# Optimization experiments

Measured on AMD Instinct MI355X. Metric: run time of the kernel, lower is better.

Reference implementation:

```python
import jax, jax.numpy as jnp
import numpy as np

D_H = 128
N_RBF = 16
R_MIN = 0.0
R_MAX = float(np.sqrt(2.0))


def _rbf(r):
    # Gaussian RBF expansion: centers linspace(R_MIN, R_MAX, N_RBF),
    # width = center spacing, exp(-(r-mu)^2 / (2*width^2))
    centers = jnp.linspace(R_MIN, R_MAX, N_RBF, dtype=r.dtype)
    width = (R_MAX - R_MIN) / (N_RBF - 1)
    gamma = 1.0 / (2.0 * width * width)
    return jnp.exp(-gamma * (r[:, None] - centers[None, :]) ** 2)


def setup_inputs() -> dict:
    key = jax.random.key(0)
    ks = jax.random.split(key, 16)
    N, E = 50000, 800000
    h = jax.random.normal(ks[0], (N, D_H), dtype=jnp.float32)
    x = jax.random.uniform(ks[1], (N, 2), dtype=jnp.float32)
    edge_index = jax.random.randint(ks[2], (2, E), 0, N, dtype=jnp.int64)
    edge_weight = jax.random.uniform(ks[3], (E,), dtype=jnp.float32)

    def lin(k, fan_in, fan_out):
        s = 1.0 / np.sqrt(fan_in)
        kw, kb = jax.random.split(k)
        W = jax.random.uniform(kw, (fan_in, fan_out), minval=-s, maxval=s, dtype=jnp.float32)
        b = jax.random.uniform(kb, (fan_out,), minval=-s, maxval=s, dtype=jnp.float32)
        return W, b

    Wm1, bm1 = lin(ks[4], 2 * D_H + N_RBF, D_H)
    Wm2, bm2 = lin(ks[5], D_H, D_H)
    Wh1, bh1 = lin(ks[6], 2 * D_H, D_H)
    Wh2, bh2 = lin(ks[7], D_H, D_H)
    ln_g = jnp.ones((D_H,), dtype=jnp.float32)
    ln_b = jnp.zeros((D_H,), dtype=jnp.float32)
    return {"h": h, "x": x, "edge_index": edge_index, "edge_weight": edge_weight,
            "Wm1": Wm1, "bm1": bm1, "Wm2": Wm2, "bm2": bm2,
            "Wh1": Wh1, "bh1": bh1, "Wh2": Wh2, "bh2": bh2,
            "ln_g": ln_g, "ln_b": ln_b}


def reference(h, x, edge_index, edge_weight, Wm1, bm1, Wm2, bm2, Wh1, bh1, Wh2, bh2, ln_g, ln_b):
    N = h.shape[0]
    src = edge_index[0]
    dst = edge_index[1]
    # per-edge geometry
    dx = x[src, :2] - x[dst, :2]                      # [E,2]
    r = jnp.sqrt(jnp.sum(dx * dx, axis=-1) + 1e-8)    # [E]
    rbf = _rbf(r)                                     # [E,n_rbf]
    # message MLP: Linear -> SiLU -> Linear
    m_in = jnp.concatenate([h[src], h[dst], rbf], axis=-1)  # [E, 2*d_h+n_rbf]
    m = jax.nn.silu(m_in @ Wm1 + bm1) @ Wm2 + bm2            # [E, d_h]
    m = m * edge_weight[:, None]
    # scatter-sum aggregate into destination nodes
    agg = jax.ops.segment_sum(m, dst, num_segments=N)        # [N, d_h]
    # node update MLP
    u_in = jnp.concatenate([h, agg], axis=-1)                # [N, 2*d_h]
    h_up = jax.nn.silu(u_in @ Wh1 + bh1) @ Wh2 + bh2         # [N, d_h]
    # residual + LayerNorm
    z = h + h_up
    mu = jnp.mean(z, axis=-1, keepdims=True)
    var = jnp.var(z, axis=-1, keepdims=True)
    return (z - mu) / jnp.sqrt(var + 1e-5) * ln_g + ln_b
```

## Files before the change

### kernel.cpp

```cpp
#include <hip/hip_runtime.h>
#include <hip/hip_bf16.h>
#include <math.h>

#define DH 128
#define NRBF 16
#define EB 256
#define NTAB 1025
#define SEGCAP 32

typedef unsigned short ushort_t;
typedef __attribute__((ext_vector_type(8))) short short8;
typedef __attribute__((ext_vector_type(4))) float floatx4;

__device__ __forceinline__ float silu_f(float v) {
    return v / (1.f + __expf(-v));
}
__device__ __forceinline__ unsigned pk_bf16(float lo, float hi) {
    __hip_bfloat162 h = __float22bfloat162_rn(make_float2(lo, hi));
    union { __hip_bfloat162 h2; unsigned u; } cv;
    cv.h2 = h;
    return cv.u;
}
__device__ __forceinline__ ushort_t f2bf1(float f) {
    unsigned u = __float_as_uint(f);
    u += 0x7FFFu + ((u >> 16) & 1u);
    return (ushort_t)(u >> 16);
}
__device__ __forceinline__ float bflo(unsigned u) { return __uint_as_float(u << 16); }
__device__ __forceinline__ float bfhi(unsigned u) { return __uint_as_float(u & 0xffff0000u); }
__device__ __forceinline__ float bf2f(ushort_t u) { return __uint_as_float(((unsigned)u) << 16); }

__device__ __forceinline__ int detect64(const int* __restrict__ ei) {
    int z = 0;
#pragma unroll
    for (int i = 0; i < 8; ++i) z |= ei[2 * i + 1];
    return (z == 0) ? 1 : 0;
}
__device__ __forceinline__ int load_dst(const int* ei, int is64, int e, int E) {
    return is64 ? ei[2 * E + 2 * e] : ei[E + e];
}
__device__ __forceinline__ int load_src(const int* ei, int is64, int e, int E) {
    return is64 ? ei[2 * e] : ei[e];
}

__global__ __launch_bounds__(256) void k_hist_prep(
    const int* __restrict__ ei, int* __restrict__ counts, int E,
    const float* __restrict__ Wm1, const float* __restrict__ Wm2,
    const float* __restrict__ Wh1, const float* __restrict__ Wh2,
    ushort_t* __restrict__ Tbf, ushort_t* __restrict__ W2f,
    ushort_t* __restrict__ W1mf, ushort_t* __restrict__ W1hf,
    ushort_t* __restrict__ W2hf, int nb_hist)
{
    const int b = blockIdx.x, tid = threadIdx.x;
    if (b < nb_hist) {
        const int e = b * 256 + tid;
        if (e < E) {
            const int is64 = detect64(ei);
            atomicAdd(&counts[load_dst(ei, is64, e, E)], 1);
        }
        return;
    }
    int b2 = b - nb_hist;
    if (b2 < 257) {
        const int i = b2 * 4 + (tid >> 6);
        if (i < NTAB) {
            const float WIDTH = 0.09428090415820634f;
            const float GAMMA = 56.25f;
            const float DELTA = 1.4142135623730951f / 1024.0f;
            const float r = (float)i * DELTA;
            const int c0 = (tid & 63) * 2;
            float a0 = 0.f, a1 = 0.f;
#pragma unroll
            for (int q = 0; q < NRBF; ++q) {
                const float dr = r - (float)q * WIDTH;
                const float w = __expf(-GAMMA * dr * dr);
                a0 = fmaf(w, Wm1[(256 + q) * DH + c0], a0);
                a1 = fmaf(w, Wm1[(256 + q) * DH + c0 + 1], a1);
            }
            *(unsigned*)(Tbf + (size_t)i * DH + c0) = pk_bf16(a0, a1);
        }
        return;
    }
    b2 -= 257;
    if (b2 < 8) {
        const int u = b2 * 256 + tid;
        const int col = u & 127, kclg = u >> 7;
        const int lg = kclg & 3, kc = kclg >> 2;
        unsigned o[4];
#pragma unroll
        for (int j = 0; j < 2; ++j) {
            o[j]     = pk_bf16(Wm2[(kc * 32 + 4 * lg + 2 * j) * DH + col],
                               Wm2[(kc * 32 + 4 * lg + 2 * j + 1) * DH + col]);
            o[2 + j] = pk_bf16(Wm2[(kc * 32 + 16 + 4 * lg + 2 * j) * DH + col],
                               Wm2[(kc * 32 + 16 + 4 * lg + 2 * j + 1) * DH + col]);
        }
        *(uint4*)(W2f + 8 * u) = make_uint4(o[0], o[1], o[2], o[3]);
        return;
    }
    b2 -= 8;
    if (b2 < 16) {
        const int u = b2 * 256 + tid;
        const int c = u & 255, kclg = u >> 8;
        const int lg = kclg & 3, kc = kclg >> 2;
        const int base = (c < 128) ? 0 : 128;
        const int cc = c & 127;
        unsigned o[4];
#pragma unroll
        for (int j = 0; j < 2; ++j) {
            o[j]     = pk_bf16(Wm1[(base + kc * 32 + 4 * lg + 2 * j) * DH + cc],
                               Wm1[(base + kc * 32 + 4 * lg + 2 * j + 1) * DH + cc]);
            o[2 + j] = pk_bf16(Wm1[(base + kc * 32 + 16 + 4 * lg + 2 * j) * DH + cc],
                               Wm1[(base + kc * 32 + 16 + 4 * lg + 2 * j + 1) * DH + cc]);
        }
        *(uint4*)(W1mf + 8 * u) = make_uint4(o[0], o[1], o[2], o[3]);
        return;
    }
    b2 -= 16;
    if (b2 < 16) {
        const int u = b2 * 256 + tid;
        const int col = u & 127, kclg = u >> 7;
        const int lg = kclg & 3, kc = kclg >> 2;
        unsigned o[4];
#pragma unroll
        for (int j = 0; j < 2; ++j) {
            o[j]     = pk_bf16(Wh1[(kc * 32 + 4 * lg + 2 * j) * DH + col],
                               Wh1[(kc * 32 + 4 * lg + 2 * j + 1) * DH + col]);
            o[2 + j] = pk_bf16(Wh1[(kc * 32 + 16 + 4 * lg + 2 * j) * DH + col],
                               Wh1[(kc * 32 + 16 + 4 * lg + 2 * j + 1) * DH + col]);
        }
        *(uint4*)(W1hf + 8 * u) = make_uint4(o[0], o[1], o[2], o[3]);
        return;
    }
    b2 -= 16;
    {
        const int u = b2 * 256 + tid;
        const int col = u & 127, kclg = u >> 7;
        const int lg = kclg & 3, kc = kclg >> 2;
        unsigned o[4];
#pragma unroll
        for (int j = 0; j < 2; ++j) {
            o[j]     = pk_bf16(Wh2[(kc * 32 + 4 * lg + 2 * j) * DH + col],
                               Wh2[(kc * 32 + 4 * lg + 2 * j + 1) * DH + col]);
            o[2 + j] = pk_bf16(Wh2[(kc * 32 + 16 + 4 * lg + 2 * j) * DH + col],
                               Wh2[(kc * 32 + 16 + 4 * lg + 2 * j + 1) * DH + col]);
        }
        *(uint4*)(W2hf + 8 * u) = make_uint4(o[0], o[1], o[2], o[3]);
    }
}

__global__ __launch_bounds__(1024) void k_scan(const int* __restrict__ counts,
                                               int* __restrict__ cursor, int N) {
    __shared__ int wsum[16];
    __shared__ int sCarry;
    const int tid = threadIdx.x, lane = tid & 63, wid = tid >> 6;
    if (tid == 0) sCarry = 0;
    __syncthreads();
    for (int c0 = 0; c0 < N; c0 += 4096) {
        const int idx = c0 + tid * 4;
        int4 v = make_int4(0, 0, 0, 0);
        if (idx < N) v = *(const int4*)(counts + idx);
        const int t01 = v.x + v.y;
        const int t012 = t01 + v.z;
        const int tot = t012 + v.w;
        int incl = tot;
#pragma unroll
        for (int d = 1; d < 64; d <<= 1) {
            int t = __shfl_up(incl, d, 64);
            if (lane >= d) incl += t;
        }
        if (lane == 63) wsum[wid] = incl;
        __syncthreads();
        if (wid == 0) {
            int s = (lane < 16) ? wsum[lane] : 0;
#pragma unroll
            for (int d = 1; d < 16; d <<= 1) {
                int t = __shfl_up(s, d, 64);
                if (lane >= d) s += t;
            }
            if (lane < 16) wsum[lane] = s;
        }
        __syncthreads();
        const int ex = sCarry + (wid > 0 ? wsum[wid - 1] : 0) + incl - tot;
        if (idx + 3 < N) {
            *(int4*)(cursor + idx) = make_int4(ex, ex + v.x, ex + t01, ex + t012);
        } else if (idx < N) {
            cursor[idx] = ex;
            if (idx + 1 < N) cursor[idx + 1] = ex + v.x;
            if (idx + 2 < N) cursor[idx + 2] = ex + t01;
        }
        __syncthreads();
        if (tid == 0) sCarry += wsum[15];
        __syncthreads();
    }
}

__global__ __launch_bounds__(256) void k_scatter_pre(
    const int* __restrict__ ei, const float* __restrict__ ew, const float* __restrict__ x,
    int* __restrict__ cursor, uint4* __restrict__ epk,
    int E, int pack,
    const float* __restrict__ h, const float* __restrict__ bm1,
    const ushort_t* __restrict__ W1mf,
    ushort_t* __restrict__ Abf, ushort_t* __restrict__ Bbf, int N, int nb_scat)
{
    const int tid = threadIdx.x;

    if ((int)blockIdx.x < nb_scat) {
        const int e = blockIdx.x * 256 + tid;
        if (e < E) {
            const int is64 = detect64(ei);
            const int s = load_src(ei, is64, e, E);
            const int d = load_dst(ei, is64, e, E);
            const int pos = atomicAdd(&cursor[d], 1);
            unsigned x0 = (unsigned)s;
            if (pack) {
                const float2 xs = *(const float2*)(x + 2 * s);
                const float2 xd = *(const float2*)(x + 2 * d);
                const float dxv = xs.x - xd.x, dyv = xs.y - xd.y;
                const float r = sqrtf(dxv * dxv + dyv * dyv + 1e-8f);
                int ti = (int)(r * 724.0773439350246f + 0.5f);
                ti = min(ti, NTAB - 1);
                x0 |= ((unsigned)ti << 16);
            }
            epk[pos] = make_uint4(x0, __float_as_uint(ew[e]), (unsigned)d, 0u);
        }
        return;
    }

    __shared__ __align__(16) ushort_t sIn[64 * DH];
    const int nblk = ((int)blockIdx.x - nb_scat) * 64;

    {
        const int row = tid >> 2, q = tid & 3;
        const int gn = nblk + row;
        const float4* ps = (const float4*)(h + (size_t)gn * DH + 32 * q);
        uint4* rowp = (uint4*)(sIn + row * DH);
        const int swz = row & 7;
#pragma unroll
        for (int i = 0; i < 4; ++i) {
            uint4 o = make_uint4(0, 0, 0, 0);
            if (gn < N) {
                const float4 g0 = ps[2 * i], g1 = ps[2 * i + 1];
                o.x = pk_bf16(g0.x, g0.y); o.y = pk_bf16(g0.z, g0.w);
                o.z = pk_bf16(g1.x, g1.y); o.w = pk_bf16(g1.z, g1.w);
            }
            rowp[(4 * q + i) ^ swz] = o;
        }
    }
    __syncthreads();

    const int lane = tid & 63, wv = tid >> 6;
    const int lr = lane & 15, lg = lane >> 4;
    const int m0l = wv * 16;

    union FragU { unsigned u[4]; short8 s8; };
    floatx4 acc[16];
#pragma unroll
    for (int ni = 0; ni < 16; ++ni) acc[ni] = (floatx4){0.f, 0.f, 0.f, 0.f};

#pragma unroll
    for (int kc = 0; kc < 4; ++kc) {
        const int b1 = 64 * kc + 8 * lg;
        const int b2 = b1 + 32;
        const int row = m0l + lr;
        const char* rbase = (const char*)(sIn + row * DH);
        const int swz = (row & 7) << 4;
        FragU af;
        const uint2 lo = *(const uint2*)(rbase + ((b1 & ~15) ^ swz) + (b1 & 15));
        const uint2 hi = *(const uint2*)(rbase + ((b2 & ~15) ^ swz) + (b2 & 15));
        af.u[0] = lo.x; af.u[1] = lo.y; af.u[2] = hi.x; af.u[3] = hi.y;
        const ushort_t* wbase = W1mf + ((size_t)(kc * 4 + lg) * 256 + lr) * 8;
        __builtin_amdgcn_s_setprio(1);
#pragma unroll
        for (int ni = 0; ni < 16; ++ni) {
            const short8 bf = *(const short8*)(wbase + ni * 128);
            acc[ni] = __builtin_amdgcn_mfma_f32_16x16x32_bf16(af.s8, bf, acc[ni], 0, 0, 0);
        }
        __builtin_amdgcn_s_setprio(0);
    }

    float bm1v[8];
#pragma unroll
    for (int ni = 0; ni < 8; ++ni) bm1v[ni] = bm1[ni * 16 + lr];
#pragma unroll
    for (int r = 0; r < 4; ++r) {
        const int gn = nblk + m0l + 4 * lg + r;
        if (gn < N) {
#pragma unroll
            for (int ni = 0; ni < 8; ++ni)
                Abf[(size_t)gn * DH + ni * 16 + lr] = f2bf1(acc[ni][r] + bm1v[ni]);
#pragma unroll
            for (int ni = 8; ni < 16; ++ni)
                Bbf[(size_t)gn * DH + (ni - 8) * 16 + lr] = f2bf1(acc[ni][r]);
        }
    }
}

__global__ __launch_bounds__(256, 4) void k_edge(
    const float* __restrict__ x, const int* __restrict__ ei, const float* __restrict__ ew,
    const uint4* __restrict__ epk,
    const ushort_t* __restrict__ W2f, const float* __restrict__ bm2,
    const ushort_t* __restrict__ Abf, const ushort_t* __restrict__ Bbf,
    const ushort_t* __restrict__ Tbf, float* __restrict__ agg,
    int sorted, int pack, int N, int E)
{
    __shared__ __align__(16) ushort_t sHid[4][16 * DH];
    __shared__ __align__(16) float ldsAgg[SEGCAP][DH];
    __shared__ int   sSrc[EB];
    __shared__ int   sDst[EB];
    __shared__ int   sLid[EB];
    __shared__ int   sTi[EB];
    __shared__ float sEw[EB];
    __shared__ int   sSegStart[SEGCAP];
    __shared__ int   sNseg;
    __shared__ int   sWtot[4];

    const int tid  = threadIdx.x;
    const int lane = tid & 63;
    const int wv   = tid >> 6;
    const int lr   = lane & 15;
    const int lg   = lane >> 4;
    const int e4   = lane >> 2;
    const int q    = lane & 3;
    const int wbase = wv * 64;

    const int nwg = gridDim.x;
    const int xcd = blockIdx.x & 7;
    const int cidx = blockIdx.x >> 3;
    const int qch = nwg >> 3, rch = nwg & 7;
    const int bid = (xcd < rch) ? (xcd * (qch + 1) + cidx)
                                : (rch * (qch + 1) + (xcd - rch) * qch + cidx);
    const int e0 = bid * EB;

    {
        const float4 z = make_float4(0.f, 0.f, 0.f, 0.f);
        float4* za = (float4*)&ldsAgg[0][0];
#pragma unroll
        for (int i = 0; i < 4; ++i) za[tid + 256 * i] = z;
    }

    {
        const int slot = e0 + tid;
        int s = 0, d = 0, ti = 0;
        float w = 0.f;
        if (slot < E) {
            if (sorted) {
                const uint4 v = epk[slot];
                w = __uint_as_float(v.y);
                d = (int)v.z;
                if (pack) { s = (int)(v.x & 0xFFFFu); ti = (int)(v.x >> 16); }
                else {
                    s = (int)v.x;
                    const float2 xs = *(const float2*)(x + 2 * s);
                    const float2 xd = *(const float2*)(x + 2 * d);
                    const float dxv = xs.x - xd.x, dyv = xs.y - xd.y;
                    const float r = sqrtf(dxv * dxv + dyv * dyv + 1e-8f);
                    ti = min((int)(r * 724.0773439350246f + 0.5f), NTAB - 1);
                }
            } else {
                const int is64 = detect64(ei);
                s = load_src(ei, is64, slot, E);
                d = load_dst(ei, is64, slot, E);
                w = ew[slot];
                const float2 xs = *(const float2*)(x + 2 * s);
                const float2 xd = *(const float2*)(x + 2 * d);
                const float dxv = xs.x - xd.x, dyv = xs.y - xd.y;
                const float r = sqrtf(dxv * dxv + dyv * dyv + 1e-8f);
                ti = min((int)(r * 724.0773439350246f + 0.5f), NTAB - 1);
            }
        } else {
            d = sorted ? (int)epk[E - 1].z : load_dst(ei, detect64(ei), E - 1, E);
        }
        sSrc[tid] = s; sDst[tid] = d; sEw[tid] = w; sTi[tid] = ti;
    }
    __syncthreads();

    {
        const int bflag = (tid > 0) && (sDst[tid] != sDst[tid - 1]);
        int incl = bflag;
#pragma unroll
        for (int dd = 1; dd < 64; dd <<= 1) {
            int t = __shfl_up(incl, dd, 64);
            if (lane >= dd) incl += t;
        }
        if (lane == 63) sWtot[wv] = incl;
        __syncthreads();
        int off = 0;
#pragma unroll
        for (int wq = 0; wq < 3; ++wq)
            if (wq < wv) off += sWtot[wq];
        incl += off;
        sLid[tid] = incl;
        if ((bflag || tid == 0) && incl < SEGCAP) sSegStart[incl] = tid;
        if (tid == EB - 1) sNseg = incl + 1;
    }
    __syncthreads();

    float bc8[8];
#pragma unroll
    for (int ni = 0; ni < 8; ++ni) bc8[ni] = bm2[ni * 16 + lr];

    union FragU { unsigned u[4]; short8 s8; };
    ushort_t* slice = &sHid[wv][0];
    floatx4 acc[8];

#pragma unroll
    for (int st = 0; st < 4; ++st) {
        const int sb = wbase + st * 16;

        const int le = sb + e4;
        const int s  = sSrc[le];
        const int d  = sDst[le];
        const int ti = sTi[le];
        const uint4* pA = (const uint4*)(Abf + (size_t)s * DH + 32 * q);
        const uint4* pB = (const uint4*)(Bbf + (size_t)d * DH + 32 * q);
        const uint4* pT = (const uint4*)(Tbf + (size_t)ti * DH + 32 * q);
        uint4 av[4], bv[4], tv[4];
#pragma unroll
        for (int i = 0; i < 4; ++i) { av[i] = pA[i]; bv[i] = pB[i]; tv[i] = pT[i]; }

        {
            uint4* rowp = (uint4*)(slice + e4 * DH);
            const int swzw = e4 & 7;
#pragma unroll
            for (int i = 0; i < 4; ++i) {
                const uint4 a = av[i]; const uint4 b = bv[i]; const uint4 t = tv[i];
                const float v0 = bflo(a.x) + bflo(b.x) + bflo(t.x);
                const float v1 = bfhi(a.x) + bfhi(b.x) + bfhi(t.x);
                const float v2 = bflo(a.y) + bflo(b.y) + bflo(t.y);
                const float v3 = bfhi(a.y) + bfhi(b.y) + bfhi(t.y);
                const float v4 = bflo(a.z) + bflo(b.z) + bflo(t.z);
                const float v5 = bfhi(a.z) + bfhi(b.z) + bfhi(t.z);
                const float v6 = bflo(a.w) + bflo(b.w) + bflo(t.w);
                const float v7 = bfhi(a.w) + bfhi(b.w) + bfhi(t.w);
                uint4 pk;
                pk.x = pk_bf16(silu_f(v0), silu_f(v1));
                pk.y = pk_bf16(silu_f(v2), silu_f(v3));
                pk.z = pk_bf16(silu_f(v4), silu_f(v5));
                pk.w = pk_bf16(silu_f(v6), silu_f(v7));
                rowp[(4 * q + i) ^ swzw] = pk;
            }
        }

#pragma unroll
        for (int ni = 0; ni < 8; ++ni) acc[ni] = (floatx4){0.f, 0.f, 0.f, 0.f};
#pragma unroll
        for (int kc = 0; kc < 4; ++kc) {
            const int bo1 = 64 * kc + 8 * lg;
            const int bo2 = bo1 + 32;
            const char* rbase = (const char*)(slice + lr * DH);
            const int swzf = (lr & 7) << 4;
            FragU af;
            const uint2 lo = *(const uint2*)(rbase + ((bo1 & ~15) ^ swzf) + (bo1 & 15));
            const uint2 hi = *(const uint2*)(rbase + ((bo2 & ~15) ^ swzf) + (bo2 & 15));
            af.u[0] = lo.x; af.u[1] = lo.y; af.u[2] = hi.x; af.u[3] = hi.y;
            const ushort_t* wb2 = W2f + ((size_t)(kc * 4 + lg) * 128 + lr) * 8;
            __builtin_amdgcn_s_setprio(1);
#pragma unroll
            for (int ni = 0; ni < 8; ++ni) {
                const short8 bf = *(const short8*)(wb2 + ni * 128);
                acc[ni] = __builtin_amdgcn_mfma_f32_16x16x32_bf16(af.s8, bf, acc[ni], 0, 0, 0);
            }
            __builtin_amdgcn_s_setprio(0);
        }

        {
            const int sbg = sb + 4 * lg;
            int lid4[4]; float ew4[4];
#pragma unroll
            for (int r = 0; r < 4; ++r) { lid4[r] = sLid[sbg + r]; ew4[r] = sEw[sbg + r]; }
#pragma unroll
            for (int ni = 0; ni < 8; ++ni) {
                const int col = ni * 16 + lr;
                const float bc = bc8[ni];
                int cur = lid4[0], curSlot = sbg;
                float avv = (acc[ni][0] + bc) * ew4[0];
#pragma unroll
                for (int r = 1; r < 4; ++r) {
                    const int l2 = lid4[r];
                    const float v = (acc[ni][r] + bc) * ew4[r];
                    if (l2 == cur) avv += v;
                    else {
                        if (cur < SEGCAP) atomicAdd(&ldsAgg[cur][col], avv);
                        else atomicAdd(agg + (size_t)sDst[curSlot] * DH + col, avv);
                        cur = l2; curSlot = sbg + r; avv = v;
                    }
                }
                if (cur < SEGCAP) atomicAdd(&ldsAgg[cur][col], avv);
                else atomicAdd(agg + (size_t)sDst[curSlot] * DH + col, avv);
            }
        }
    }

    __syncthreads();

    const int ns = sNseg;
    const int gmax = (ns < SEGCAP) ? ns : SEGCAP;
    for (int idx = tid; idx < (gmax << 7); idx += 256) {
        const int g = idx >> 7, col = idx & 127;
        const float v = ldsAgg[g][col];
        const int dst = sDst[sSegStart[g]];
        float* p = agg + (size_t)dst * DH + col;
        if (sorted && g > 0 && g < ns - 1) *p = v;
        else atomicAdd(p, v);
    }
}

__global__ __launch_bounds__(256) void k_node(
    const float* __restrict__ h, const float* __restrict__ agg,
    const ushort_t* __restrict__ W1hf, const float* __restrict__ bh1,
    const ushort_t* __restrict__ W2hf, const float* __restrict__ bh2,
    const float* __restrict__ ln_g, const float* __restrict__ ln_b,
    float* __restrict__ out, int N)
{
    __shared__ __align__(16) ushort_t sIn[64 * 256];
    __shared__ __align__(16) ushort_t sHid[64 * DH];
    const int tid = threadIdx.x;
    const int nblk = blockIdx.x * 64;

    {
        const int row = tid >> 2, q = tid & 3;
        const int gn = nblk + row;
        const float4* ps = (q < 2) ? (const float4*)(h + (size_t)gn * DH + 64 * q)
                                   : (const float4*)(agg + (size_t)gn * DH + 64 * (q - 2));
        uint4* rowp = (uint4*)(sIn + row * 256);
        const int swz = row & 7;
#pragma unroll
        for (int i = 0; i < 8; ++i) {
            uint4 o = make_uint4(0, 0, 0, 0);
            if (gn < N) {
                const float4 g0 = ps[2 * i], g1 = ps[2 * i + 1];
                o.x = pk_bf16(g0.x, g0.y); o.y = pk_bf16(g0.z, g0.w);
                o.z = pk_bf16(g1.x, g1.y); o.w = pk_bf16(g1.z, g1.w);
            }
            rowp[(8 * q + i) ^ swz] = o;
        }
    }
    __syncthreads();

    const int lane = tid & 63, wv = tid >> 6;
    const int lr = lane & 15, lg = lane >> 4;
    const int m0l = wv * 16;

    union FragU { unsigned u[4]; short8 s8; };

    floatx4 acc[8];
#pragma unroll
    for (int ni = 0; ni < 8; ++ni) acc[ni] = (floatx4){0.f, 0.f, 0.f, 0.f};

#pragma unroll
    for (int kc = 0; kc < 8; ++kc) {
        const int b1 = 64 * kc + 8 * lg;
        const int b2 = b1 + 32;
        const int row = m0l + lr;
        const char* rbase = (const char*)(sIn + row * 256);
        const int swz = (row & 7) << 4;
        FragU af;
        const uint2 lo = *(const uint2*)(rbase + ((b1 & ~15) ^ swz) + (b1 & 15));
        const uint2 hi = *(const uint2*)(rbase + ((b2 & ~15) ^ swz) + (b2 & 15));
        af.u[0] = lo.x; af.u[1] = lo.y; af.u[2] = hi.x; af.u[3] = hi.y;
        const ushort_t* wbase = W1hf + ((size_t)(kc * 4 + lg) * 128 + lr) * 8;
        __builtin_amdgcn_s_setprio(1);
#pragma unroll
        for (int ni = 0; ni < 8; ++ni) {
            const short8 bf = *(const short8*)(wbase + ni * 128);
            acc[ni] = __builtin_amdgcn_mfma_f32_16x16x32_bf16(af.s8, bf, acc[ni], 0, 0, 0);
        }
        __builtin_amdgcn_s_setprio(0);
    }

    {
        float bh1v[8];
#pragma unroll
        for (int ni = 0; ni < 8; ++ni) bh1v[ni] = bh1[ni * 16 + lr];
#pragma unroll
        for (int r = 0; r < 4; ++r) {
            const int row = m0l + 4 * lg + r;
            const int swz = row & 7;
            ushort_t* rp = sHid + row * DH;
#pragma unroll
            for (int ni = 0; ni < 8; ++ni) {
                const int col = ni * 16 + lr;
                rp[(((col >> 3) ^ swz) << 3) + (col & 7)] =
                    f2bf1(silu_f(acc[ni][r] + bh1v[ni]));
            }
        }
    }

    floatx4 acc2[8];
#pragma unroll
    for (int ni = 0; ni < 8; ++ni) acc2[ni] = (floatx4){0.f, 0.f, 0.f, 0.f};

#pragma unroll
    for (int kc = 0; kc < 4; ++kc) {
        const int b1 = 64 * kc + 8 * lg;
        const int b2 = b1 + 32;
        const int row = m0l + lr;
        const char* rbase = (const char*)(sHid + row * DH);
        const int swz = (row & 7) << 4;
        FragU af;
        const uint2 lo = *(const uint2*)(rbase + ((b1 & ~15) ^ swz) + (b1 & 15));
        const uint2 hi = *(const uint2*)(rbase + ((b2 & ~15) ^ swz) + (b2 & 15));
        af.u[0] = lo.x; af.u[1] = lo.y; af.u[2] = hi.x; af.u[3] = hi.y;
        const ushort_t* wbase = W2hf + ((size_t)(kc * 4 + lg) * 128 + lr) * 8;
        __builtin_amdgcn_s_setprio(1);
#pragma unroll
        for (int ni = 0; ni < 8; ++ni) {
            const short8 bf = *(const short8*)(wbase + ni * 128);
            acc2[ni] = __builtin_amdgcn_mfma_f32_16x16x32_bf16(af.s8, bf, acc2[ni], 0, 0, 0);
        }
        __builtin_amdgcn_s_setprio(0);
    }

    float gv[8], bv[8], b2v[8];
#pragma unroll
    for (int ni = 0; ni < 8; ++ni) {
        const int col = ni * 16 + lr;
        gv[ni] = ln_g[col]; bv[ni] = ln_b[col]; b2v[ni] = bh2[col];
    }
#pragma unroll
    for (int r = 0; r < 4; ++r) {
        const int row = m0l + 4 * lg + r;
        const int gn = nblk + row;
        const int swz = row & 7;
        float z[8];
        float s1 = 0.f, s2 = 0.f;
#pragma unroll
        for (int ni = 0; ni < 8; ++ni) {
            const int col = ni * 16 + lr;
            const float hv = bf2f(sIn[row * 256 + (((col >> 3) ^ swz) << 3) + (col & 7)]);
            z[ni] = acc2[ni][r] + b2v[ni] + hv;
            s1 += z[ni]; s2 += z[ni] * z[ni];
        }
#pragma unroll
        for (int m = 1; m < 16; m <<= 1) {
            s1 += __shfl_xor(s1, m, 64);
            s2 += __shfl_xor(s2, m, 64);
        }
        const float mean = s1 * (1.f / 128.f);
        const float var = s2 * (1.f / 128.f) - mean * mean;
        const float rstd = rsqrtf(var + 1e-5f);
        if (gn < N) {
#pragma unroll
            for (int ni = 0; ni < 8; ++ni) {
                const int col = ni * 16 + lr;
                out[(size_t)gn * DH + col] = (z[ni] - mean) * rstd * gv[ni] + bv[ni];
            }
        }
    }
}

extern "C" void kernel_launch(void* const* d_in, const int* in_sizes, int n_in,
                              void* d_out, int out_size, void* d_ws, size_t ws_size,
                              hipStream_t stream)
{
    (void)n_in; (void)out_size;
    const float* h   = (const float*)d_in[0];
    const float* x   = (const float*)d_in[1];
    const int*   ei  = (const int*)d_in[2];
    const float* ew  = (const float*)d_in[3];
    const float* Wm1 = (const float*)d_in[4];
    const float* bm1 = (const float*)d_in[5];
    const float* Wm2 = (const float*)d_in[6];
    const float* bm2 = (const float*)d_in[7];
    const float* Wh1 = (const float*)d_in[8];
    const float* bh1 = (const float*)d_in[9];
    const float* Wh2 = (const float*)d_in[10];
    const float* bh2 = (const float*)d_in[11];
    const float* lng = (const float*)d_in[12];
    const float* lnb = (const float*)d_in[13];
    float* out = (float*)d_out;

    const int N = in_sizes[0] / DH;
    const int E = in_sizes[3];

    float*    agg  = (float*)d_ws;
    int*   counts  = (int*)(agg + (size_t)N * DH);
    int*   cursor  = counts + N;
    ushort_t* Abf  = (ushort_t*)((((uintptr_t)(cursor + N)) + 15) & ~(uintptr_t)15);
    ushort_t* Bbf  = Abf + (size_t)N * DH;
    ushort_t* W2f  = Bbf + (size_t)N * DH;
    ushort_t* Tbf  = W2f + 16384;
    ushort_t* W1mf = Tbf + (size_t)NTAB * DH;
    ushort_t* W1hf = W1mf + 32768;
    ushort_t* W2hf = W1hf + 32768;
    uint4* epk     = (uint4*)((((uintptr_t)(W2hf + 16384)) + 15) & ~(uintptr_t)15);

    const size_t need = ((char*)(epk + E)) - ((char*)d_ws);
    const int use_sort = (ws_size >= need) ? 1 : 0;
    const int pack = use_sort && (N <= 65535);

    const int nb_hist = use_sort ? (E + 255) / 256 : 0;
    const int nb_prep = 257 + 8 + 16 + 16 + 8;
    const int nb_scat = nb_hist;
    const int nb_pre  = (N + 63) / 64;

    hipMemsetAsync(agg, 0, (size_t)N * DH * sizeof(float) + (use_sort ? (size_t)N * 4 : 0), stream);
    k_hist_prep<<<nb_hist + nb_prep, 256, 0, stream>>>(ei, counts, E, Wm1, Wm2, Wh1, Wh2,
                                                       Tbf, W2f, W1mf, W1hf, W2hf, nb_hist);
    if (use_sort)
        k_scan<<<1, 1024, 0, stream>>>(counts, cursor, N);
    k_scatter_pre<<<nb_scat + nb_pre, 256, 0, stream>>>(ei, ew, x, cursor, epk, E, pack,
                                                        h, bm1, W1mf, Abf, Bbf, N, nb_scat);
    k_edge<<<(E + EB - 1) / EB, 256, 0, stream>>>(x, ei, ew, epk,
                                                  W2f, bm2, Abf, Bbf, Tbf, agg,
                                                  use_sort, pack, N, E);
    k_node<<<(N + 63) / 64, 256, 0, stream>>>(h, agg, W1hf, bh1, W2hf, bh2, lng, lnb, out, N);
}
```

Before: 403.7 us.

## Split edge kernel into gather/SiLU build pass and MFMA GEMM-scatter pass

The fused edge kernel is split in two. A build kernel gathers the bf16 A/B/RBF-table rows per edge, applies SiLU, and writes a swizzled bf16 hidden matrix to workspace. A GEMM kernel then loads those rows into LDS, runs the second-layer MFMA, and does the segmented scatter-add, with an XCD-aware block remap. The goal is to decouple the latency-bound random gathers from the MFMA/atomic phase so each runs at better occupancy. The cost is an extra E×128 bf16 write and read through global memory, about 200MB of traffic. The fused kernel is kept as a fallback when the workspace is too small, and its launch bounds change from 4 to 2.

```diff
diff --git a/kernel.cpp b/kernel.cpp
--- a/kernel.cpp
+++ b/kernel.cpp
@@ -295,7 +295,221 @@
     }
 }
 
-__global__ __launch_bounds__(256, 4) void k_edge(
+__global__ __launch_bounds__(256) void k_build(
+    const float* __restrict__ x, const uint4* __restrict__ epk,
+    const ushort_t* __restrict__ Abf, const ushort_t* __restrict__ Bbf,
+    const ushort_t* __restrict__ Tbf, ushort_t* __restrict__ Hbf,
+    int pack, int E)
+{
+    const int gid = blockIdx.x * 256 + threadIdx.x;
+    const int e = gid >> 2, q = gid & 3;
+    if (e >= E) return;
+
+    const uint4 v = epk[e];
+    const int d = (int)v.z;
+    int s, ti;
+    if (pack) { s = (int)(v.x & 0xFFFFu); ti = (int)(v.x >> 16); }
+    else {
+        s = (int)v.x;
+        const float2 xs = *(const float2*)(x + 2 * s);
+        const float2 xd = *(const float2*)(x + 2 * d);
+        const float dxv = xs.x - xd.x, dyv = xs.y - xd.y;
+        const float r = sqrtf(dxv * dxv + dyv * dyv + 1e-8f);
+        ti = min((int)(r * 724.0773439350246f + 0.5f), NTAB - 1);
+    }
+
+    const uint4* pA = (const uint4*)(Abf + (size_t)s * DH + 32 * q);
+    const uint4* pB = (const uint4*)(Bbf + (size_t)d * DH + 32 * q);
+    const uint4* pT = (const uint4*)(Tbf + (size_t)ti * DH + 32 * q);
+    uint4 av[4], bv[4], tv[4];
+#pragma unroll
+    for (int i = 0; i < 4; ++i) { av[i] = pA[i]; bv[i] = pB[i]; tv[i] = pT[i]; }
+
+    uint4* rowp = (uint4*)(Hbf + (size_t)e * DH);
+    const int swz = e & 7;
+#pragma unroll
+    for (int i = 0; i < 4; ++i) {
+        const uint4 a = av[i]; const uint4 b = bv[i]; const uint4 t = tv[i];
+        const float v0 = bflo(a.x) + bflo(b.x) + bflo(t.x);
+        const float v1 = bfhi(a.x) + bfhi(b.x) + bfhi(t.x);
+        const float v2 = bflo(a.y) + bflo(b.y) + bflo(t.y);
+        const float v3 = bfhi(a.y) + bfhi(b.y) + bfhi(t.y);
+        const float v4 = bflo(a.z) + bflo(b.z) + bflo(t.z);
+        const float v5 = bfhi(a.z) + bfhi(b.z) + bfhi(t.z);
+        const float v6 = bflo(a.w) + bflo(b.w) + bflo(t.w);
+        const float v7 = bfhi(a.w) + bfhi(b.w) + bfhi(t.w);
+        uint4 pk;
+        pk.x = pk_bf16(silu_f(v0), silu_f(v1));
+        pk.y = pk_bf16(silu_f(v2), silu_f(v3));
+        pk.z = pk_bf16(silu_f(v4), silu_f(v5));
+        pk.w = pk_bf16(silu_f(v6), silu_f(v7));
+        rowp[(4 * q + i) ^ swz] = pk;
+    }
+}
+
+__global__ __launch_bounds__(256, 4) void k_gemm(
+    const uint4* __restrict__ epk, const ushort_t* __restrict__ Hbf,
+    const ushort_t* __restrict__ W2f, const float* __restrict__ bm2,
+    float* __restrict__ agg, int N, int E)
+{
+    __shared__ __align__(16) ushort_t sHid[4][16 * DH];
+    __shared__ __align__(16) float ldsAgg[SEGCAP][DH];
+    __shared__ int   sDst[EB];
+    __shared__ int   sLid[EB];
+    __shared__ float sEw[EB];
+    __shared__ int   sSegStart[SEGCAP];
+    __shared__ int   sNseg;
+    __shared__ int   sWtot[4];
+
+    const int tid  = threadIdx.x;
+    const int lane = tid & 63;
+    const int wv   = tid >> 6;
+    const int lr   = lane & 15;
+    const int lg   = lane >> 4;
+    const int e4   = lane >> 2;
+    const int q    = lane & 3;
+    const int wbase = wv * 64;
+
+    const int nwg = gridDim.x;
+    const int xcd = blockIdx.x & 7;
+    const int cidx = blockIdx.x >> 3;
+    const int qch = nwg >> 3, rch = nwg & 7;
+    const int bid = (xcd < rch) ? (xcd * (qch + 1) + cidx)
+                                : (rch * (qch + 1) + (xcd - rch) * qch + cidx);
+    const int e0 = bid * EB;
+
+    {
+        const float4 z = make_float4(0.f, 0.f, 0.f, 0.f);
+        float4* za = (float4*)&ldsAgg[0][0];
+#pragma unroll
+        for (int i = 0; i < 4; ++i) za[tid + 256 * i] = z;
+    }
+
+    {
+        const int slot = e0 + tid;
+        int d;
+        float w = 0.f;
+        if (slot < E) {
+            const uint4 v = epk[slot];
+            w = __uint_as_float(v.y);
+            d = (int)v.z;
+        } else {
+            d = (int)epk[E - 1].z;
+        }
+        sDst[tid] = d; sEw[tid] = w;
+    }
+    __syncthreads();
+
+    {
+        const int bflag = (tid > 0) && (sDst[tid] != sDst[tid - 1]);
+        int incl = bflag;
+#pragma unroll
+        for (int dd = 1; dd < 64; dd <<= 1) {
+            int t = __shfl_up(incl, dd, 64);
+            if (lane >= dd) incl += t;
+        }
+        if (lane == 63) sWtot[wv] = incl;
+        __syncthreads();
+        int off = 0;
+#pragma unroll
+        for (int wq = 0; wq < 3; ++wq)
+            if (wq < wv) off += sWtot[wq];
+        incl += off;
+        sLid[tid] = incl;
+        if ((bflag || tid == 0) && incl < SEGCAP) sSegStart[incl] = tid;
+        if (tid == EB - 1) sNseg = incl + 1;
+    }
+    __syncthreads();
+
+    float bc8[8];
+#pragma unroll
+    for (int ni = 0; ni < 8; ++ni) bc8[ni] = bm2[ni * 16 + lr];
+
+    union FragU { unsigned u[4]; short8 s8; };
+    ushort_t* slice = &sHid[wv][0];
+    floatx4 acc[8];
+
+#pragma unroll
+    for (int st = 0; st < 4; ++st) {
+        const int sb = wbase + st * 16;
+        const int le = sb + e4;
+
+        {
+            const uint4* gsrc = (const uint4*)(Hbf + (size_t)(e0 + le) * DH);
+            uint4* rowp = (uint4*)(slice + e4 * DH);
+            const int swz = e4 & 7;
+#pragma unroll
+            for (int i = 0; i < 4; ++i) {
+                const int c = (4 * q + i) ^ swz;
+                rowp[c] = gsrc[c];
+            }
+        }
+
+#pragma unroll
+        for (int ni = 0; ni < 8; ++ni) acc[ni] = (floatx4){0.f, 0.f, 0.f, 0.f};
+#pragma unroll
+        for (int kc = 0; kc < 4; ++kc) {
+            const int bo1 = 64 * kc + 8 * lg;
+            const int bo2 = bo1 + 32;
+            const char* rbase = (const char*)(slice + lr * DH);
+            const int swzf = (lr & 7) << 4;
+            FragU af;
+            const uint2 lo = *(const uint2*)(rbase + ((bo1 & ~15) ^ swzf) + (bo1 & 15));
+            const uint2 hi = *(const uint2*)(rbase + ((bo2 & ~15) ^ swzf) + (bo2 & 15));
+            af.u[0] = lo.x; af.u[1] = lo.y; af.u[2] = hi.x; af.u[3] = hi.y;
+            const ushort_t* wb2 = W2f + ((size_t)(kc * 4 + lg) * 128 + lr) * 8;
+            __builtin_amdgcn_s_setprio(1);
+#pragma unroll
+            for (int ni = 0; ni < 8; ++ni) {
+                const short8 bf = *(const short8*)(wb2 + ni * 128);
+                acc[ni] = __builtin_amdgcn_mfma_f32_16x16x32_bf16(af.s8, bf, acc[ni], 0, 0, 0);
+            }
+            __builtin_amdgcn_s_setprio(0);
+        }
+
+        {
+            const int sbg = sb + 4 * lg;
+            int lid4[4]; float ew4[4];
+#pragma unroll
+            for (int r = 0; r < 4; ++r) { lid4[r] = sLid[sbg + r]; ew4[r] = sEw[sbg + r]; }
+#pragma unroll
+            for (int ni = 0; ni < 8; ++ni) {
+                const int col = ni * 16 + lr;
+                const float bc = bc8[ni];
+                int cur = lid4[0], curSlot = sbg;
+                float avv = (acc[ni][0] + bc) * ew4[0];
+#pragma unroll
+                for (int r = 1; r < 4; ++r) {
+                    const int l2 = lid4[r];
+                    const float v = (acc[ni][r] + bc) * ew4[r];
+                    if (l2 == cur) avv += v;
+                    else {
+                        if (cur < SEGCAP) atomicAdd(&ldsAgg[cur][col], avv);
+                        else atomicAdd(agg + (size_t)sDst[curSlot] * DH + col, avv);
+                        cur = l2; curSlot = sbg + r; avv = v;
+                    }
+                }
+                if (cur < SEGCAP) atomicAdd(&ldsAgg[cur][col], avv);
+                else atomicAdd(agg + (size_t)sDst[curSlot] * DH + col, avv);
+            }
+        }
+    }
+
+    __syncthreads();
+
+    const int ns = sNseg;
+    const int gmax = (ns < SEGCAP) ? ns : SEGCAP;
+    for (int idx = tid; idx < (gmax << 7); idx += 256) {
+        const int g = idx >> 7, col = idx & 127;
+        const float v = ldsAgg[g][col];
+        const int dst = sDst[sSegStart[g]];
+        float* p = agg + (size_t)dst * DH + col;
+        if (g > 0 && g < ns - 1) *p = v;
+        else atomicAdd(p, v);
+    }
+}
+
+__global__ __launch_bounds__(256, 2) void k_edge_mono(
     const float* __restrict__ x, const int* __restrict__ ei, const float* __restrict__ ew,
     const uint4* __restrict__ epk,
     const ushort_t* __restrict__ W2f, const float* __restrict__ bm2,
@@ -406,7 +620,6 @@
 #pragma unroll
     for (int st = 0; st < 4; ++st) {
         const int sb = wbase + st * 16;
-
         const int le = sb + e4;
         const int s  = sSrc[le];
         const int d  = sDst[le];
@@ -672,6 +885,7 @@
 
     const int N = in_sizes[0] / DH;
     const int E = in_sizes[3];
+    const int nbE = (E + EB - 1) / EB;
 
     float*    agg  = (float*)d_ws;
     int*   counts  = (int*)(agg + (size_t)N * DH);
@@ -684,9 +898,12 @@
     ushort_t* W1hf = W1mf + 32768;
     ushort_t* W2hf = W1hf + 32768;
     uint4* epk     = (uint4*)((((uintptr_t)(W2hf + 16384)) + 15) & ~(uintptr_t)15);
-
-    const size_t need = ((char*)(epk + E)) - ((char*)d_ws);
-    const int use_sort = (ws_size >= need) ? 1 : 0;
+    ushort_t* Hbf  = (ushort_t*)(epk + E);
+
+    const size_t need_sort  = ((char*)(epk + E)) - ((char*)d_ws);
+    const size_t need_split = need_sort + (size_t)nbE * EB * DH * sizeof(ushort_t);
+    const int use_sort  = (ws_size >= need_sort) ? 1 : 0;
+    const int use_split = use_sort && (ws_size >= need_split);
     const int pack = use_sort && (N <= 65535);
 
     const int nb_hist = use_sort ? (E + 255) / 256 : 0;
@@ -701,8 +918,12 @@
         k_scan<<<1, 1024, 0, stream>>>(counts, cursor, N);
     k_scatter_pre<<<nb_scat + nb_pre, 256, 0, stream>>>(ei, ew, x, cursor, epk, E, pack,
                                                         h, bm1, W1mf, Abf, Bbf, N, nb_scat);
-    k_edge<<<(E + EB - 1) / EB, 256, 0, stream>>>(x, ei, ew, epk,
-                                                  W2f, bm2, Abf, Bbf, Tbf, agg,
-                                                  use_sort, pack, N, E);
+    if (use_split) {
+        k_build<<<(4 * E + 255) / 256, 256, 0, stream>>>(x, epk, Abf, Bbf, Tbf, Hbf, pack, E);
+        k_gemm<<<nbE, 256, 0, stream>>>(epk, Hbf, W2f, bm2, agg, N, E);
+    } else {
+        k_edge_mono<<<nbE, 256, 0, stream>>>(x, ei, ew, epk, W2f, bm2, Abf, Bbf, Tbf, agg,
+                                             use_sort, pack, N, E);
+    }
     k_node<<<(N + 63) / 64, 256, 0, stream>>>(h, agg, W1hf, bh1, W2hf, bh2, lng, lnb, out, N);
 }
```

Result: faster. 385.0 us (-4.6%).
